# Performance work log

Hardware: AMD Instinct MI355X
Metric: run time of the kernel (lower is better)

## Reference

```python
import jax, jax.numpy as jnp
import numpy as np

T, B, N, DIN, H = 64, 32, 64, 128, 128  # seq_len, batch, num_nodes, input_dim, hid_dim
NUM_LAYERS = 2


def _make_cell_params(key, din):
    k1, k2, k3, k4 = jax.random.split(key, 4)
    s = 0.05
    Wg = jax.random.normal(k1, (2 * (din + H), 2 * H), jnp.float32) * s  # gates (r,u)
    bg = jnp.zeros((2 * H,), jnp.float32)
    Wc = jax.random.normal(k2, (2 * (din + H), H), jnp.float32) * s      # candidate
    bc = jnp.zeros((H,), jnp.float32)
    Wq = jax.random.normal(k3, (H, H), jnp.float32) * s                  # graph learner q
    Wk = jax.random.normal(k4, (H, H), jnp.float32) * s                  # graph learner k
    return Wg, bg, Wc, bc, Wq, Wk


def setup_inputs() -> dict:
    key = jax.random.key(0)
    k_in, k_sup, k_l0, k_l1 = jax.random.split(key, 4)
    inputs = jax.random.normal(k_in, (T, B, N, DIN), jnp.float32)
    initial_hidden_state = jnp.zeros((NUM_LAYERS, B, N * H), jnp.float32)
    supports = jax.nn.softmax(jax.random.normal(k_sup, (B, N, N), jnp.float32), axis=-1)
    Wg0, bg0, Wc0, bc0, Wq0, Wk0 = _make_cell_params(k_l0, DIN)
    Wg1, bg1, Wc1, bc1, Wq1, Wk1 = _make_cell_params(k_l1, H)
    return dict(inputs=inputs, initial_hidden_state=initial_hidden_state, supports=supports,
                Wg0=Wg0, bg0=bg0, Wc0=Wc0, bc0=bc0, Wq0=Wq0, Wk0=Wk0,
                Wg1=Wg1, bg1=bg1, Wc1=Wc1, bc1=bc1, Wq1=Wq1, Wk1=Wk1)


def _cell_step(params, supports, x, h):
    # x: (B, N, din), h: (B, N, H), supports: (B, N, N)
    Wg, bg, Wc, bc, Wq, Wk = params
    xh = jnp.concatenate([x, h], axis=-1)
    conv = jnp.einsum('bnm,bmd->bnd', supports, xh)                # graph conv
    gates = jax.nn.sigmoid(jnp.concatenate([xh, conv], -1) @ Wg + bg)
    r, u = jnp.split(gates, 2, axis=-1)
    xh_r = jnp.concatenate([x, r * h], axis=-1)
    conv_c = jnp.einsum('bnm,bmd->bnd', supports, xh_r)
    c = jnp.tanh(jnp.concatenate([xh_r, conv_c], -1) @ Wc + bc)
    h_new = u * h + (1.0 - u) * c
    # dynamic graph learner: new adjacency from the updated hidden state
    scores = jnp.einsum('bnd,bmd->bnm', h_new @ Wq, h_new @ Wk)
    new_supports = jax.nn.softmax(jax.nn.relu(scores), axis=-1)
    return h_new, new_supports


def _run_layer(params, x_seq, h0, supports, din):
    # x_seq: (T, B, N*din) -> hidden sequence (T, B, N, H)
    def step(carry, x_t):
        h, sup = carry
        h_new, sup_new = _cell_step(params, sup, x_t.reshape(B, N, din), h)
        return (h_new, sup_new), h_new
    (h_last, sup_last), hs = jax.lax.scan(step, (h0.reshape(B, N, H), supports), x_seq)
    return hs, h_last, sup_last


def reference(inputs, initial_hidden_state, supports,
              Wg0, bg0, Wc0, bc0, Wq0, Wk0,
              Wg1, bg1, Wc1, bc1, Wq1, Wk1):
    layer_params = [(Wg0, bg0, Wc0, bc0, Wq0, Wk0), (Wg1, bg1, Wc1, bc1, Wq1, Wk1)]
    dins = [DIN, H]
    cur = inputs.reshape(T, B, N * DIN)
    sup = supports
    out_hidden = []
    for i in range(NUM_LAYERS):
        hs, h_last, sup = _run_layer(layer_params[i], cur, initial_hidden_state[i], sup, dins[i])
        out_hidden.append(h_last.reshape(B, N * H))
        cur = hs.reshape(T, B, N * H)
    output_hidden = jnp.stack(out_hidden, axis=0)   # (num_layers, B, N*H)
    return output_hidden, cur                        # cur: (T, B, N*H)
```

## Files before the change

### kernel.cpp

```cpp
#include <hip/hip_runtime.h>

#define TT 64
#define BB 32
#define NN 64
#define HH 128
#define NH 8192

using short8 = __attribute__((ext_vector_type(8))) short;
using f32x16 = __attribute__((ext_vector_type(16))) float;

__device__ __forceinline__ unsigned short f2bf(float f) {
  unsigned int u = __float_as_uint(f);
  u = (u + 0x7FFFu + ((u >> 16) & 1u)) >> 16;
  return (unsigned short)u;
}
__device__ __forceinline__ float bf2f(unsigned short s) {
  return __uint_as_float(((unsigned int)s) << 16);
}
__device__ __forceinline__ float sigm(float x) { return 1.0f / (1.0f + __expf(-x)); }
__device__ __forceinline__ float tanh_fast(float x) { return 2.0f / (1.0f + __expf(-2.0f * x)) - 1.0f; }

__device__ __forceinline__ uint2 pack4(float a, float b, float c, float d) {
  uint2 r;
  r.x = (unsigned int)f2bf(a) | ((unsigned int)f2bf(b) << 16);
  r.y = (unsigned int)f2bf(c) | ((unsigned int)f2bf(d) << 16);
  return r;
}
__device__ __forceinline__ short8 ldsfrag(const unsigned short* p) {
  union { uint2 u2[2]; short8 s; } f;
  f.u2[0] = *(const uint2*)p;
  f.u2[1] = *(const uint2*)(p + 4);
  return f.s;
}
__device__ __forceinline__ short8 ldgfrag(const unsigned short* p) {
  union { uint4 u4; short8 s; } f;
  f.u4 = *(const uint4*)p;
  return f.s;
}

__global__ void sglc_pack(const float* __restrict__ Wg0, const float* __restrict__ Wc0,
                          const float* __restrict__ Wq0, const float* __restrict__ Wk0,
                          const float* __restrict__ Wg1, const float* __restrict__ Wc1,
                          const float* __restrict__ Wq1, const float* __restrict__ Wk1,
                          unsigned short* __restrict__ dst) {
  int idx = blockIdx.x * 256 + threadIdx.x;
  if (idx >= 458752) return;
  int layer = idx / 229376;
  int lo = idx - layer * 229376;
  const float* src; int nkc, ncshift, off;
  if (lo < 131072)      { src = layer ? Wg1 : Wg0; nkc = 32; ncshift = 8; off = 0; }
  else if (lo < 196608) { src = layer ? Wc1 : Wc0; nkc = 32; ncshift = 7; off = 131072; }
  else if (lo < 212992) { src = layer ? Wq1 : Wq0; nkc = 8;  ncshift = 7; off = 196608; }
  else                  { src = layer ? Wk1 : Wk0; nkc = 8;  ncshift = 7; off = 212992; }
  int l2 = lo - off;
  int k = l2 >> ncshift;
  int c = l2 & ((1 << ncshift) - 1);
  int c32 = c >> 5, n32 = c & 31;
  int kc = k >> 4, kl = k & 15;
  int half = kl >> 3, j = kl & 7;
  int lane = half * 32 + n32;
  int dstoff = layer * 229376 + off + (((c32 * nkc + kc) << 9) + lane * 8 + j);
  dst[dstoff] = f2bf(src[(size_t)k * (1 << ncshift) + c]);
}

#define SX_O   0
#define SH_O   8448
#define SRH_O  16896
#define SQ_O   25344
#define SK_O   33792
#define SSUP_O 42240
#define SPT_O  46592
#define LDS_USHORTS 64000

extern "C" __global__ void __launch_bounds__(1024, 4)
sglc_main(const float* __restrict__ Xin, const float* __restrict__ H0,
          const float* __restrict__ Sup0,
          const float* __restrict__ bg0, const float* __restrict__ bc0,
          const float* __restrict__ bg1, const float* __restrict__ bc1,
          const unsigned short* __restrict__ Wp, float* __restrict__ Out) {
  extern __shared__ unsigned short sm[];
  unsigned short* sX   = sm + SX_O;
  unsigned short* sHb  = sm + SH_O;
  unsigned short* sRH  = sm + SRH_O;
  unsigned short* sQ   = sm + SQ_O;
  unsigned short* sK   = sm + SK_O;
  unsigned short* sSup = sm + SSUP_O;
  unsigned short* sPT  = sm + SPT_O;
  float* sS = (float*)(sm + SPT_O);

  const int b = blockIdx.x;
  const int tid = threadIdx.x;
  const int lane = tid & 63;
  const int w = tid >> 6;
  const int n32 = lane & 31;
  const int half = lane >> 5;
  const int kob = half * 8;

  float* OutH = Out;
  float* Cur  = Out + 2 * BB * NH;

  float h_reg[32];

  for (int layer = 0; layer < 2; ++layer) {
    const int Lw = layer * 229376;
    const float* bg = layer ? bg1 : bg0;
    const float* bc = layer ? bc1 : bc0;
    const float* xbase = layer ? Cur : Xin;
    const float* h0p = H0 + (size_t)(layer * BB + b) * NH;

    const float bgv = (w < 8) ? bg[(w & 7) * 32 + n32] : 0.0f;
    const float bcv = (w >= 4 && w < 8) ? bc[(w - 4) * 32 + n32] : 0.0f;

    {
      int r = tid >> 4, c0 = (tid & 15) * 8;
      const float* hp = h0p + r * 128 + c0;
      float4 v0 = *(const float4*)(hp);
      float4 v1 = *(const float4*)(hp + 4);
      *(uint2*)(sHb + r * 132 + c0)     = pack4(v0.x, v0.y, v0.z, v0.w);
      *(uint2*)(sHb + r * 132 + c0 + 4) = pack4(v1.x, v1.y, v1.z, v1.w);
      const float* xp = xbase + (size_t)(0 * BB + b) * NH + r * 128 + c0;
      float4 x0 = *(const float4*)(xp);
      float4 x1 = *(const float4*)(xp + 4);
      *(uint2*)(sX + r * 132 + c0)     = pack4(x0.x, x0.y, x0.z, x0.w);
      *(uint2*)(sX + r * 132 + c0 + 4) = pack4(x1.x, x1.y, x1.z, x1.w);
      if (layer == 0) {
        int rs = tid >> 4, cs = (tid & 15) * 4;
        float4 sv = *(const float4*)(Sup0 + (size_t)b * 4096 + rs * 64 + cs);
        *(uint2*)(sSup + rs * 68 + cs) = pack4(sv.x, sv.y, sv.z, sv.w);
      }
    }
    if (w >= 4 && w < 8) {
      const int col = (w - 4) * 32 + n32;
#pragma unroll
      for (int tt = 0; tt < 2; ++tt)
#pragma unroll
        for (int g = 0; g < 4; ++g)
#pragma unroll
          for (int i = 0; i < 4; ++i)
            h_reg[tt * 16 + 4 * g + i] = h0p[(tt * 32 + 8 * g + 4 * half + i) * 128 + col];
    }
    __syncthreads();

    for (int t = 0; t < TT; ++t) {
      union { float u[32]; short8 bq[8]; } su_;
      f32x16 acc0, acc1;
#pragma unroll
      for (int z = 0; z < 16; ++z) { acc0[z] = 0.0f; acc1[z] = 0.0f; }

      {
        const int c32g = w & 7;
        const unsigned short* wb = Wp + Lw + (((c32g * 32 + (w < 8 ? 0 : 16)) << 9) + lane * 8);
#pragma unroll
        for (int kc = 0; kc < 16; ++kc) {
          const unsigned short* asrc = (kc < 8) ? (sX + kc * 16 + kob) : (sHb + (kc - 8) * 16 + kob);
          short8 a0 = ldsfrag(asrc + n32 * 132);
          short8 a1 = ldsfrag(asrc + (32 + n32) * 132);
          short8 bf = ldgfrag(wb + (kc << 9));
          acc0 = __builtin_amdgcn_mfma_f32_32x32x16_bf16(a0, bf, acc0, 0, 0, 0);
          acc1 = __builtin_amdgcn_mfma_f32_32x32x16_bf16(a1, bf, acc1, 0, 0, 0);
        }
        if (w >= 8) {
          unsigned short* pb = sPT + (c32g * 32 + n32) * 68;
#pragma unroll
          for (int tt = 0; tt < 2; ++tt) {
            const f32x16& ac = tt ? acc1 : acc0;
#pragma unroll
            for (int g = 0; g < 4; ++g)
              *(uint2*)(pb + tt * 32 + 8 * g + 4 * half) =
                  pack4(ac[4 * g], ac[4 * g + 1], ac[4 * g + 2], ac[4 * g + 3]);
          }
        }
      }
      __syncthreads();

      if (w < 8) {
        const int c32g = w & 7;
#pragma unroll
        for (int kc2 = 0; kc2 < 4; ++kc2) {
          short8 a0 = ldsfrag(sSup + n32 * 68 + kc2 * 16 + kob);
          short8 a1 = ldsfrag(sSup + (32 + n32) * 68 + kc2 * 16 + kob);
          short8 bf = ldsfrag(sPT + (c32g * 32 + n32) * 68 + kc2 * 16 + kob);
          acc0 = __builtin_amdgcn_mfma_f32_32x32x16_bf16(a0, bf, acc0, 0, 0, 0);
          acc1 = __builtin_amdgcn_mfma_f32_32x32x16_bf16(a1, bf, acc1, 0, 0, 0);
        }
        const int col = (w & 7) * 32 + n32;
        if (w < 4) {
#pragma unroll
          for (int tt = 0; tt < 2; ++tt) {
            const f32x16& ac = tt ? acc1 : acc0;
#pragma unroll
            for (int g = 0; g < 4; ++g)
#pragma unroll
              for (int i = 0; i < 4; ++i) {
                int row = tt * 32 + 8 * g + 4 * half + i;
                float rv = sigm(ac[4 * g + i] + bgv);
                float hv = bf2f(sHb[row * 132 + col]);
                sRH[row * 132 + col] = f2bf(rv * hv);
              }
          }
        } else {
#pragma unroll
          for (int tt = 0; tt < 2; ++tt) {
            const f32x16& ac = tt ? acc1 : acc0;
#pragma unroll
            for (int g = 0; g < 4; ++g)
#pragma unroll
              for (int i = 0; i < 4; ++i)
                su_.u[tt * 16 + 4 * g + i] = sigm(ac[4 * g + i] + bgv);
          }
        }
      } else {
        const unsigned short* qb =
            Wp + Lw + ((w < 12) ? 196608 : 212992) + ((((w - 8) & 3) * 8) << 9) + lane * 8;
#pragma unroll
        for (int kc = 0; kc < 8; ++kc) su_.bq[kc] = ldgfrag(qb + (kc << 9));
      }
      __syncthreads();

      f32x16 ca0, ca1;
#pragma unroll
      for (int z = 0; z < 16; ++z) { ca0[z] = 0.0f; ca1[z] = 0.0f; }
      if (w >= 4 && w < 12) {
        const int c32c = (w < 8) ? (w - 4) : (w - 8);
        const unsigned short* wb = Wp + Lw + 131072 + (((c32c * 32 + (w < 8 ? 0 : 16)) << 9) + lane * 8);
#pragma unroll
        for (int kc = 0; kc < 16; ++kc) {
          const unsigned short* asrc = (kc < 8) ? (sX + kc * 16 + kob) : (sRH + (kc - 8) * 16 + kob);
          short8 a0 = ldsfrag(asrc + n32 * 132);
          short8 a1 = ldsfrag(asrc + (32 + n32) * 132);
          short8 bf = ldgfrag(wb + (kc << 9));
          ca0 = __builtin_amdgcn_mfma_f32_32x32x16_bf16(a0, bf, ca0, 0, 0, 0);
          ca1 = __builtin_amdgcn_mfma_f32_32x32x16_bf16(a1, bf, ca1, 0, 0, 0);
        }
        if (w >= 8) {
          unsigned short* pb = sPT + (c32c * 32 + n32) * 68;
#pragma unroll
          for (int tt = 0; tt < 2; ++tt) {
            const f32x16& ac = tt ? ca1 : ca0;
#pragma unroll
            for (int g = 0; g < 4; ++g)
              *(uint2*)(pb + tt * 32 + 8 * g + 4 * half) =
                  pack4(ac[4 * g], ac[4 * g + 1], ac[4 * g + 2], ac[4 * g + 3]);
          }
        }
      }
      __syncthreads();

      if (w >= 4 && w < 8) {
        const int c32c = w - 4;
        const int col = c32c * 32 + n32;
#pragma unroll
        for (int kc2 = 0; kc2 < 4; ++kc2) {
          short8 a0 = ldsfrag(sSup + n32 * 68 + kc2 * 16 + kob);
          short8 a1 = ldsfrag(sSup + (32 + n32) * 68 + kc2 * 16 + kob);
          short8 bf = ldsfrag(sPT + col * 68 + kc2 * 16 + kob);
          ca0 = __builtin_amdgcn_mfma_f32_32x32x16_bf16(a0, bf, ca0, 0, 0, 0);
          ca1 = __builtin_amdgcn_mfma_f32_32x32x16_bf16(a1, bf, ca1, 0, 0, 0);
        }
        float* curp = Cur + (size_t)(t * BB + b) * NH;
        float* outp = OutH + (size_t)(layer * BB + b) * NH;
#pragma unroll
        for (int tt = 0; tt < 2; ++tt) {
          const f32x16& ac = tt ? ca1 : ca0;
#pragma unroll
          for (int g = 0; g < 4; ++g)
#pragma unroll
            for (int i = 0; i < 4; ++i) {
              int r16 = tt * 16 + 4 * g + i;
              float cv = tanh_fast(ac[4 * g + i] + bcv);
              float uv = su_.u[r16];
              float hn = uv * h_reg[r16] + (1.0f - uv) * cv;
              h_reg[r16] = hn;
              int row = tt * 32 + 8 * g + 4 * half + i;
              sHb[row * 132 + col] = f2bf(hn);
              curp[row * 128 + col] = hn;
              if (t == TT - 1) outp[row * 128 + col] = hn;
            }
        }
      } else if (w < 4 || w >= 12) {
        if (t < TT - 1) {
          const float* xn = xbase + (size_t)((t + 1) * BB + b) * NH;
          int sidx = (w < 4 ? w : w - 8) * 64 + lane;
          int r = sidx >> 3, c0 = (sidx & 7) * 16;
          const float* sp = xn + r * 128 + c0;
          unsigned short* dp = sX + r * 132 + c0;
#pragma unroll
          for (int q4 = 0; q4 < 4; ++q4) {
            float4 v = *(const float4*)(sp + q4 * 4);
            *(uint2*)(dp + q4 * 4) = pack4(v.x, v.y, v.z, v.w);
          }
        }
      }
      __syncthreads();

      if (w >= 8) {
        const int col = ((w - 8) & 3) * 32 + n32;
        f32x16 qa0, qa1;
#pragma unroll
        for (int z = 0; z < 16; ++z) { qa0[z] = 0.0f; qa1[z] = 0.0f; }
#pragma unroll
        for (int kc = 0; kc < 8; ++kc) {
          short8 a0 = ldsfrag(sHb + n32 * 132 + kc * 16 + kob);
          short8 a1 = ldsfrag(sHb + (32 + n32) * 132 + kc * 16 + kob);
          qa0 = __builtin_amdgcn_mfma_f32_32x32x16_bf16(a0, su_.bq[kc], qa0, 0, 0, 0);
          qa1 = __builtin_amdgcn_mfma_f32_32x32x16_bf16(a1, su_.bq[kc], qa1, 0, 0, 0);
        }
        unsigned short* dstm = (w < 12) ? sQ : sK;
#pragma unroll
        for (int tt = 0; tt < 2; ++tt) {
          const f32x16& ac = tt ? qa1 : qa0;
#pragma unroll
          for (int g = 0; g < 4; ++g)
#pragma unroll
            for (int i = 0; i < 4; ++i)
              dstm[(tt * 32 + 8 * g + 4 * half + i) * 132 + col] = f2bf(ac[4 * g + i]);
        }
      }
      __syncthreads();

      if (w < 4) {
        const int rt = w & 1, ct = w >> 1;
        f32x16 sa;
#pragma unroll
        for (int z = 0; z < 16; ++z) sa[z] = 0.0f;
#pragma unroll
        for (int kc = 0; kc < 8; ++kc) {
          short8 a0 = ldsfrag(sQ + (rt * 32 + n32) * 132 + kc * 16 + kob);
          short8 bf = ldsfrag(sK + (ct * 32 + n32) * 132 + kc * 16 + kob);
          sa = __builtin_amdgcn_mfma_f32_32x32x16_bf16(a0, bf, sa, 0, 0, 0);
        }
#pragma unroll
        for (int g = 0; g < 4; ++g)
#pragma unroll
          for (int i = 0; i < 4; ++i)
            sS[(rt * 32 + 8 * g + 4 * half + i) * 66 + ct * 32 + n32] = fmaxf(sa[4 * g + i], 0.0f);
      }
      __syncthreads();

      {
        int row = tid >> 4, ci = (tid & 15) * 4;
        float2 v01 = *(const float2*)(sS + row * 66 + ci);
        float2 v23 = *(const float2*)(sS + row * 66 + ci + 2);
        float s0 = v01.x, s1 = v01.y, s2 = v23.x, s3 = v23.y;
        float mx = fmaxf(fmaxf(s0, s1), fmaxf(s2, s3));
#pragma unroll
        for (int off = 1; off < 16; off <<= 1) mx = fmaxf(mx, __shfl_xor(mx, off, 16));
        float e0 = __expf(s0 - mx), e1 = __expf(s1 - mx);
        float e2 = __expf(s2 - mx), e3 = __expf(s3 - mx);
        float sum = e0 + e1 + e2 + e3;
#pragma unroll
        for (int off = 1; off < 16; off <<= 1) sum += __shfl_xor(sum, off, 16);
        float inv = 1.0f / sum;
        *(uint2*)(sSup + row * 68 + ci) = pack4(e0 * inv, e1 * inv, e2 * inv, e3 * inv);
      }
      __syncthreads();
    }
    __syncthreads();
  }
}

extern "C" void kernel_launch(void* const* d_in, const int* in_sizes, int n_in,
                              void* d_out, int out_size, void* d_ws, size_t ws_size,
                              hipStream_t stream) {
  const float* Xin  = (const float*)d_in[0];
  const float* H0   = (const float*)d_in[1];
  const float* Sup0 = (const float*)d_in[2];
  const float* Wg0  = (const float*)d_in[3];
  const float* bg0  = (const float*)d_in[4];
  const float* Wc0  = (const float*)d_in[5];
  const float* bc0  = (const float*)d_in[6];
  const float* Wq0  = (const float*)d_in[7];
  const float* Wk0  = (const float*)d_in[8];
  const float* Wg1  = (const float*)d_in[9];
  const float* bg1  = (const float*)d_in[10];
  const float* Wc1  = (const float*)d_in[11];
  const float* bc1  = (const float*)d_in[12];
  const float* Wq1  = (const float*)d_in[13];
  const float* Wk1  = (const float*)d_in[14];
  unsigned short* Wp = (unsigned short*)d_ws;

  hipFuncSetAttribute(reinterpret_cast<const void*>(sglc_main),
                      hipFuncAttributeMaxDynamicSharedMemorySize, LDS_USHORTS * 2);

  hipLaunchKernelGGL(sglc_pack, dim3(1792), dim3(256), 0, stream,
                     Wg0, Wc0, Wq0, Wk0, Wg1, Wc1, Wq1, Wk1, Wp);
  hipLaunchKernelGGL(sglc_main, dim3(BB), dim3(1024), LDS_USHORTS * 2, stream,
                     Xin, H0, Sup0, bg0, bc0, bg1, bc1, Wp, (float*)d_out);
}
```

Measured before the change: 3.456 ms.

## Precompute input projections in parallel kernel and keep recurrent weights in registers

Result: slower. 3.725 ms (+7.8%).

```diff
diff --git a/kernel.cpp b/kernel.cpp
--- a/kernel.cpp
+++ b/kernel.cpp
@@ -3,7 +3,6 @@
 #define TT 64
 #define BB 32
 #define NN 64
-#define HH 128
 #define NH 8192
 
 using short8 = __attribute__((ext_vector_type(8))) short;
@@ -14,18 +13,18 @@
   u = (u + 0x7FFFu + ((u >> 16) & 1u)) >> 16;
   return (unsigned short)u;
 }
+__device__ __forceinline__ unsigned int pack2(float a, float b) {
+  return (unsigned int)f2bf(a) | ((unsigned int)f2bf(b) << 16);
+}
+__device__ __forceinline__ uint2 pack4(float a, float b, float c, float d) {
+  uint2 r; r.x = pack2(a, b); r.y = pack2(c, d); return r;
+}
 __device__ __forceinline__ float bf2f(unsigned short s) {
   return __uint_as_float(((unsigned int)s) << 16);
 }
 __device__ __forceinline__ float sigm(float x) { return 1.0f / (1.0f + __expf(-x)); }
 __device__ __forceinline__ float tanh_fast(float x) { return 2.0f / (1.0f + __expf(-2.0f * x)) - 1.0f; }
 
-__device__ __forceinline__ uint2 pack4(float a, float b, float c, float d) {
-  uint2 r;
-  r.x = (unsigned int)f2bf(a) | ((unsigned int)f2bf(b) << 16);
-  r.y = (unsigned int)f2bf(c) | ((unsigned int)f2bf(d) << 16);
-  return r;
-}
 __device__ __forceinline__ short8 ldsfrag(const unsigned short* p) {
   union { uint2 u2[2]; short8 s; } f;
   f.u2[0] = *(const uint2*)p;
@@ -36,6 +35,22 @@
   union { uint4 u4; short8 s; } f;
   f.u4 = *(const uint4*)p;
   return f.s;
+}
+__device__ __forceinline__ void store16(unsigned short* p, const f32x16& v) {
+  uint4 q0, q1;
+  q0.x = pack2(v[0], v[1]);   q0.y = pack2(v[2], v[3]);
+  q0.z = pack2(v[4], v[5]);   q0.w = pack2(v[6], v[7]);
+  q1.x = pack2(v[8], v[9]);   q1.y = pack2(v[10], v[11]);
+  q1.z = pack2(v[12], v[13]); q1.w = pack2(v[14], v[15]);
+  *(uint4*)p = q0; *(uint4*)(p + 8) = q1;
+}
+__device__ __forceinline__ void addinit(f32x16& a, uint4 c0, uint4 c1) {
+  unsigned int u[8] = {c0.x, c0.y, c0.z, c0.w, c1.x, c1.y, c1.z, c1.w};
+#pragma unroll
+  for (int i = 0; i < 8; ++i) {
+    a[2 * i]     += __uint_as_float(u[i] << 16);
+    a[2 * i + 1] += __uint_as_float(u[i] & 0xffff0000u);
+  }
 }
 
 __global__ void sglc_pack(const float* __restrict__ Wg0, const float* __restrict__ Wc0,
@@ -46,316 +61,356 @@
   int idx = blockIdx.x * 256 + threadIdx.x;
   if (idx >= 458752) return;
   int layer = idx / 229376;
-  int lo = idx - layer * 229376;
-  const float* src; int nkc, ncshift, off;
-  if (lo < 131072)      { src = layer ? Wg1 : Wg0; nkc = 32; ncshift = 8; off = 0; }
-  else if (lo < 196608) { src = layer ? Wc1 : Wc0; nkc = 32; ncshift = 7; off = 131072; }
-  else if (lo < 212992) { src = layer ? Wq1 : Wq0; nkc = 8;  ncshift = 7; off = 196608; }
-  else                  { src = layer ? Wk1 : Wk0; nkc = 8;  ncshift = 7; off = 212992; }
-  int l2 = lo - off;
-  int k = l2 >> ncshift;
-  int c = l2 & ((1 << ncshift) - 1);
-  int c32 = c >> 5, n32 = c & 31;
-  int kc = k >> 4, kl = k & 15;
-  int half = kl >> 3, j = kl & 7;
-  int lane = half * 32 + n32;
-  int dstoff = layer * 229376 + off + (((c32 * nkc + kc) << 9) + lane * 8 + j);
-  dst[dstoff] = f2bf(src[(size_t)k * (1 << ncshift) + c]);
-}
-
-#define SX_O   0
-#define SH_O   8448
-#define SRH_O  16896
-#define SQ_O   25344
-#define SK_O   33792
-#define SSUP_O 42240
-#define SPT_O  46592
-#define LDS_USHORTS 64000
-
-extern "C" __global__ void __launch_bounds__(1024, 4)
-sglc_main(const float* __restrict__ Xin, const float* __restrict__ H0,
-          const float* __restrict__ Sup0,
-          const float* __restrict__ bg0, const float* __restrict__ bc0,
-          const float* __restrict__ bg1, const float* __restrict__ bc1,
-          const unsigned short* __restrict__ Wp, float* __restrict__ Out) {
+  int l = idx - layer * 229376;
+  const float* Wg = layer ? Wg1 : Wg0;
+  const float* Wc = layer ? Wc1 : Wc0;
+  const float* Wq = layer ? Wq1 : Wq0;
+  const float* Wk = layer ? Wk1 : Wk0;
+  int region = (l < 98304) ? 0 : 1;
+  int l2 = region ? (l - 98304) : l;
+  int tile = l2 >> 12;
+  int rem = l2 & 4095;
+  int kc = rem >> 9, li = rem & 511;
+  int lane = li >> 3, jj = li & 7;
+  int krow = kc * 16 + (lane >> 5) * 8 + jj;
+  int col32 = lane & 31;
+  const float* src; int ld, row0, colbase;
+  if (region == 0) {
+    if (tile < 8)       { src = Wg; ld = 256; row0 = 0;   colbase = tile * 32; }
+    else if (tile < 16) { src = Wg; ld = 256; row0 = 256; colbase = (tile - 8) * 32; }
+    else if (tile < 20) { src = Wc; ld = 128; row0 = 0;   colbase = (tile - 16) * 32; }
+    else                { src = Wc; ld = 128; row0 = 256; colbase = (tile - 20) * 32; }
+  } else {
+    if (tile < 8)       { src = Wg; ld = 256; row0 = 128; colbase = tile * 32; }
+    else if (tile < 16) { src = Wg; ld = 256; row0 = 384; colbase = (tile - 8) * 32; }
+    else if (tile < 20) { src = Wc; ld = 128; row0 = 128; colbase = (tile - 16) * 32; }
+    else if (tile < 24) { src = Wc; ld = 128; row0 = 384; colbase = (tile - 20) * 32; }
+    else if (tile < 28) { src = Wq; ld = 128; row0 = 0;   colbase = (tile - 24) * 32; }
+    else                { src = Wk; ld = 128; row0 = 0;   colbase = (tile - 28) * 32; }
+  }
+  dst[idx] = f2bf(src[(size_t)(row0 + krow) * ld + colbase + col32]);
+}
+
+__global__ void __launch_bounds__(256)
+sglc_pre(const float* __restrict__ xbase, const unsigned short* __restrict__ Wpre,
+         unsigned short* __restrict__ Pinit) {
+  const int gw = blockIdx.x * 4 + (threadIdx.x >> 6);
+  const int lane = threadIdx.x & 63;
+  const int n32 = lane & 31, half = lane >> 5;
+  const int t = gw >> 5, b = gw & 31;
+  const float* xp = xbase + (size_t)(t * BB + b) * NH;
+  short8 afr[2][8];
+#pragma unroll
+  for (int rt = 0; rt < 2; ++rt)
+#pragma unroll
+    for (int kc = 0; kc < 8; ++kc) {
+      const float* s = xp + (size_t)(rt * 32 + n32) * 128 + kc * 16 + half * 8;
+      float4 v0 = *(const float4*)s;
+      float4 v1 = *(const float4*)(s + 4);
+      union { uint2 u[2]; short8 ss; } tmp;
+      tmp.u[0] = pack4(v0.x, v0.y, v0.z, v0.w);
+      tmp.u[1] = pack4(v1.x, v1.y, v1.z, v1.w);
+      afr[rt][kc] = tmp.ss;
+    }
+  unsigned short* ob = Pinit + ((size_t)(t * BB + b) * 24) * 2048;
+  for (int j = 0; j < 24; ++j) {
+    f32x16 a0, a1;
+#pragma unroll
+    for (int z = 0; z < 16; ++z) { a0[z] = 0.0f; a1[z] = 0.0f; }
+#pragma unroll
+    for (int kc = 0; kc < 8; ++kc) {
+      short8 bf = ldgfrag(Wpre + ((j * 8 + kc) << 9) + lane * 8);
+      a0 = __builtin_amdgcn_mfma_f32_32x32x16_bf16(afr[0][kc], bf, a0, 0, 0, 0);
+      a1 = __builtin_amdgcn_mfma_f32_32x32x16_bf16(afr[1][kc], bf, a1, 0, 0, 0);
+    }
+    store16(ob + (j * 2 + 0) * 1024 + lane * 16, a0);
+    store16(ob + (j * 2 + 1) * 1024 + lane * 16, a1);
+  }
+}
+
+#define SHB_O  0
+#define SRH_O  8448
+#define SSUP_O 16896
+#define SPT_O  21248
+#define SQ_O   21248
+#define SK_O   29696
+#define SS_O   38656
+#define SHF_O  47104
+#define SU_O   63744
+#define LDS_BYTES 160768
+
+__global__ void __launch_bounds__(1024, 4)
+sglc_rec(const float* __restrict__ H0l, const float* __restrict__ Sup0,
+         const unsigned short* __restrict__ SupX,
+         const float* __restrict__ bg, const float* __restrict__ bc,
+         const unsigned short* __restrict__ Wrec, const unsigned short* __restrict__ Pinit,
+         unsigned short* __restrict__ SupXout,
+         float* __restrict__ OutHl, float* __restrict__ Cur, int layer) {
   extern __shared__ unsigned short sm[];
-  unsigned short* sX   = sm + SX_O;
-  unsigned short* sHb  = sm + SH_O;
+  unsigned short* sHb  = sm + SHB_O;
   unsigned short* sRH  = sm + SRH_O;
+  unsigned short* sSup = sm + SSUP_O;
+  unsigned short* sPT  = sm + SPT_O;
   unsigned short* sQ   = sm + SQ_O;
   unsigned short* sK   = sm + SK_O;
-  unsigned short* sSup = sm + SSUP_O;
-  unsigned short* sPT  = sm + SPT_O;
-  float* sS = (float*)(sm + SPT_O);
-
-  const int b = blockIdx.x;
-  const int tid = threadIdx.x;
-  const int lane = tid & 63;
-  const int w = tid >> 6;
-  const int n32 = lane & 31;
-  const int half = lane >> 5;
-  const int kob = half * 8;
-
-  float* OutH = Out;
-  float* Cur  = Out + 2 * BB * NH;
-
-  float h_reg[32];
-
-  for (int layer = 0; layer < 2; ++layer) {
-    const int Lw = layer * 229376;
-    const float* bg = layer ? bg1 : bg0;
-    const float* bc = layer ? bc1 : bc0;
-    const float* xbase = layer ? Cur : Xin;
-    const float* h0p = H0 + (size_t)(layer * BB + b) * NH;
-
-    const float bgv = (w < 8) ? bg[(w & 7) * 32 + n32] : 0.0f;
-    const float bcv = (w >= 4 && w < 8) ? bc[(w - 4) * 32 + n32] : 0.0f;
-
+  float* sS  = (float*)(sm + SS_O);
+  float* sHf = (float*)(sm + SHF_O);
+  float* sU  = (float*)(sm + SU_O);
+
+  const int b = blockIdx.x, tid = threadIdx.x;
+  const int lane = tid & 63, w = tid >> 6;
+  const int n32 = lane & 31, half = lane >> 5, kob = half * 8;
+
+  short8 wg[8];
+#pragma unroll
+  for (int kc = 0; kc < 8; ++kc)
+    wg[kc] = ldgfrag(Wrec + ((w * 8 + kc) << 9) + lane * 8);
+
+  const float bgv = (w < 8) ? bg[w * 32 + n32] : 0.0f;
+  const float bcv = (w >= 4 && w < 8) ? bc[(w - 4) * 32 + n32] : 0.0f;
+
+  {
+    int r = tid >> 4, c0 = (tid & 15) * 8;
+    const float* hp = H0l + (size_t)b * NH + r * 128 + c0;
+    float4 v0 = *(const float4*)(hp);
+    float4 v1 = *(const float4*)(hp + 4);
+    sHf[r * 130 + c0 + 0] = v0.x; sHf[r * 130 + c0 + 1] = v0.y;
+    sHf[r * 130 + c0 + 2] = v0.z; sHf[r * 130 + c0 + 3] = v0.w;
+    sHf[r * 130 + c0 + 4] = v1.x; sHf[r * 130 + c0 + 5] = v1.y;
+    sHf[r * 130 + c0 + 6] = v1.z; sHf[r * 130 + c0 + 7] = v1.w;
+    *(uint2*)(sHb + r * 132 + c0)     = pack4(v0.x, v0.y, v0.z, v0.w);
+    *(uint2*)(sHb + r * 132 + c0 + 4) = pack4(v1.x, v1.y, v1.z, v1.w);
+    if (layer == 0) {
+      int cs = (tid & 15) * 4;
+      float4 sv = *(const float4*)(Sup0 + (size_t)b * 4096 + r * 64 + cs);
+      *(uint2*)(sSup + r * 68 + cs) = pack4(sv.x, sv.y, sv.z, sv.w);
+    } else {
+      for (int i = tid; i < 4352; i += 1024) sSup[i] = SupX[(size_t)b * 4352 + i];
+    }
+  }
+  __syncthreads();
+
+  for (int t = 0; t < TT; ++t) {
+    const size_t pbase = ((size_t)(t * BB + b) * 24) * 2048;
+
+    f32x16 acc0, acc1;
     {
-      int r = tid >> 4, c0 = (tid & 15) * 8;
-      const float* hp = h0p + r * 128 + c0;
-      float4 v0 = *(const float4*)(hp);
-      float4 v1 = *(const float4*)(hp + 4);
-      *(uint2*)(sHb + r * 132 + c0)     = pack4(v0.x, v0.y, v0.z, v0.w);
-      *(uint2*)(sHb + r * 132 + c0 + 4) = pack4(v1.x, v1.y, v1.z, v1.w);
-      const float* xp = xbase + (size_t)(0 * BB + b) * NH + r * 128 + c0;
-      float4 x0 = *(const float4*)(xp);
-      float4 x1 = *(const float4*)(xp + 4);
-      *(uint2*)(sX + r * 132 + c0)     = pack4(x0.x, x0.y, x0.z, x0.w);
-      *(uint2*)(sX + r * 132 + c0 + 4) = pack4(x1.x, x1.y, x1.z, x1.w);
-      if (layer == 0) {
-        int rs = tid >> 4, cs = (tid & 15) * 4;
-        float4 sv = *(const float4*)(Sup0 + (size_t)b * 4096 + rs * 64 + cs);
-        *(uint2*)(sSup + rs * 68 + cs) = pack4(sv.x, sv.y, sv.z, sv.w);
-      }
+      const unsigned short* pb = Pinit + pbase + (size_t)w * 2048 + lane * 16;
+      uint4 c00 = *(const uint4*)(pb);
+      uint4 c01 = *(const uint4*)(pb + 8);
+      uint4 c10 = *(const uint4*)(pb + 1024);
+      uint4 c11 = *(const uint4*)(pb + 1024 + 8);
+#pragma unroll
+      for (int z = 0; z < 16; ++z) { acc0[z] = 0.0f; acc1[z] = 0.0f; }
+#pragma unroll
+      for (int kc = 0; kc < 8; ++kc) {
+        short8 a0 = ldsfrag(sHb + n32 * 132 + kc * 16 + kob);
+        short8 a1 = ldsfrag(sHb + (32 + n32) * 132 + kc * 16 + kob);
+        acc0 = __builtin_amdgcn_mfma_f32_32x32x16_bf16(a0, wg[kc], acc0, 0, 0, 0);
+        acc1 = __builtin_amdgcn_mfma_f32_32x32x16_bf16(a1, wg[kc], acc1, 0, 0, 0);
+      }
+      addinit(acc0, c00, c01);
+      addinit(acc1, c10, c11);
+      if (w >= 8) {
+        unsigned short* pt = sPT + ((w - 8) * 32 + n32) * 68;
+#pragma unroll
+        for (int tt = 0; tt < 2; ++tt) {
+          const f32x16& ac = tt ? acc1 : acc0;
+#pragma unroll
+          for (int g = 0; g < 4; ++g)
+            *(uint2*)(pt + tt * 32 + 8 * g + 4 * half) =
+                pack4(ac[4 * g], ac[4 * g + 1], ac[4 * g + 2], ac[4 * g + 3]);
+        }
+      }
+    }
+    __syncthreads();
+
+    short8 st[8];
+    if (w >= 4 && w < 12) {
+      const int tile = w + 12;
+#pragma unroll
+      for (int kc = 0; kc < 8; ++kc)
+        st[kc] = ldgfrag(Wrec + ((tile * 8 + kc) << 9) + lane * 8);
+    }
+    if (w < 8) {
+#pragma unroll
+      for (int kc2 = 0; kc2 < 4; ++kc2) {
+        short8 a0 = ldsfrag(sSup + n32 * 68 + kc2 * 16 + kob);
+        short8 a1 = ldsfrag(sSup + (32 + n32) * 68 + kc2 * 16 + kob);
+        short8 bf = ldsfrag(sPT + (w * 32 + n32) * 68 + kc2 * 16 + kob);
+        acc0 = __builtin_amdgcn_mfma_f32_32x32x16_bf16(a0, bf, acc0, 0, 0, 0);
+        acc1 = __builtin_amdgcn_mfma_f32_32x32x16_bf16(a1, bf, acc1, 0, 0, 0);
+      }
+      const int col = w * 32 + n32;
+      if (w < 4) {
+#pragma unroll
+        for (int tt = 0; tt < 2; ++tt) {
+          const f32x16& ac = tt ? acc1 : acc0;
+#pragma unroll
+          for (int g = 0; g < 4; ++g)
+#pragma unroll
+            for (int i = 0; i < 4; ++i) {
+              int row = tt * 32 + 8 * g + 4 * half + i;
+              float rv = sigm(ac[4 * g + i] + bgv);
+              sRH[row * 132 + col] = f2bf(rv * sHf[row * 130 + col]);
+            }
+        }
+      } else {
+        const int ucol = col - 128;
+#pragma unroll
+        for (int tt = 0; tt < 2; ++tt) {
+          const f32x16& ac = tt ? acc1 : acc0;
+#pragma unroll
+          for (int g = 0; g < 4; ++g)
+#pragma unroll
+            for (int i = 0; i < 4; ++i) {
+              int row = tt * 32 + 8 * g + 4 * half + i;
+              sU[row * 130 + ucol] = sigm(ac[4 * g + i] + bgv);
+            }
+        }
+      }
+    }
+    __syncthreads();
+
+    f32x16 ca0, ca1;
+    if (w >= 4 && w < 12) {
+      const unsigned short* pb = Pinit + pbase + (size_t)(w + 12) * 2048 + lane * 16;
+      uint4 c00 = *(const uint4*)(pb);
+      uint4 c01 = *(const uint4*)(pb + 8);
+      uint4 c10 = *(const uint4*)(pb + 1024);
+      uint4 c11 = *(const uint4*)(pb + 1024 + 8);
+#pragma unroll
+      for (int z = 0; z < 16; ++z) { ca0[z] = 0.0f; ca1[z] = 0.0f; }
+#pragma unroll
+      for (int kc = 0; kc < 8; ++kc) {
+        short8 a0 = ldsfrag(sRH + n32 * 132 + kc * 16 + kob);
+        short8 a1 = ldsfrag(sRH + (32 + n32) * 132 + kc * 16 + kob);
+        ca0 = __builtin_amdgcn_mfma_f32_32x32x16_bf16(a0, st[kc], ca0, 0, 0, 0);
+        ca1 = __builtin_amdgcn_mfma_f32_32x32x16_bf16(a1, st[kc], ca1, 0, 0, 0);
+      }
+      addinit(ca0, c00, c01);
+      addinit(ca1, c10, c11);
+      if (w >= 8) {
+        unsigned short* pt = sPT + ((w - 8) * 32 + n32) * 68;
+#pragma unroll
+        for (int tt = 0; tt < 2; ++tt) {
+          const f32x16& ac = tt ? ca1 : ca0;
+#pragma unroll
+          for (int g = 0; g < 4; ++g)
+            *(uint2*)(pt + tt * 32 + 8 * g + 4 * half) =
+                pack4(ac[4 * g], ac[4 * g + 1], ac[4 * g + 2], ac[4 * g + 3]);
+        }
+      }
+    }
+    __syncthreads();
+
+    if (w < 4) {
+#pragma unroll
+      for (int kc = 0; kc < 8; ++kc)
+        st[kc] = ldgfrag(Wrec + (((24 + w) * 8 + kc) << 9) + lane * 8);
+    } else if (w >= 12) {
+#pragma unroll
+      for (int kc = 0; kc < 8; ++kc)
+        st[kc] = ldgfrag(Wrec + (((16 + w) * 8 + kc) << 9) + lane * 8);
     }
     if (w >= 4 && w < 8) {
       const int col = (w - 4) * 32 + n32;
 #pragma unroll
-      for (int tt = 0; tt < 2; ++tt)
+      for (int kc2 = 0; kc2 < 4; ++kc2) {
+        short8 a0 = ldsfrag(sSup + n32 * 68 + kc2 * 16 + kob);
+        short8 a1 = ldsfrag(sSup + (32 + n32) * 68 + kc2 * 16 + kob);
+        short8 bf = ldsfrag(sPT + ((w - 4) * 32 + n32) * 68 + kc2 * 16 + kob);
+        ca0 = __builtin_amdgcn_mfma_f32_32x32x16_bf16(a0, bf, ca0, 0, 0, 0);
+        ca1 = __builtin_amdgcn_mfma_f32_32x32x16_bf16(a1, bf, ca1, 0, 0, 0);
+      }
+      float* curp = Cur + (size_t)(t * BB + b) * NH;
+      float* outp = OutHl + (size_t)b * NH;
+#pragma unroll
+      for (int tt = 0; tt < 2; ++tt) {
+        const f32x16& ac = tt ? ca1 : ca0;
 #pragma unroll
         for (int g = 0; g < 4; ++g)
 #pragma unroll
+          for (int i = 0; i < 4; ++i) {
+            int row = tt * 32 + 8 * g + 4 * half + i;
+            float cv = tanh_fast(ac[4 * g + i] + bcv);
+            float uv = sU[row * 130 + col];
+            float hn = uv * sHf[row * 130 + col] + (1.0f - uv) * cv;
+            sHf[row * 130 + col] = hn;
+            sHb[row * 132 + col] = f2bf(hn);
+            curp[row * 128 + col] = hn;
+            if (t == TT - 1) outp[row * 128 + col] = hn;
+          }
+      }
+    }
+    __syncthreads();
+
+    if (w < 4 || w >= 12) {
+      f32x16 qa0, qa1;
+#pragma unroll
+      for (int z = 0; z < 16; ++z) { qa0[z] = 0.0f; qa1[z] = 0.0f; }
+#pragma unroll
+      for (int kc = 0; kc < 8; ++kc) {
+        short8 a0 = ldsfrag(sHb + n32 * 132 + kc * 16 + kob);
+        short8 a1 = ldsfrag(sHb + (32 + n32) * 132 + kc * 16 + kob);
+        qa0 = __builtin_amdgcn_mfma_f32_32x32x16_bf16(a0, st[kc], qa0, 0, 0, 0);
+        qa1 = __builtin_amdgcn_mfma_f32_32x32x16_bf16(a1, st[kc], qa1, 0, 0, 0);
+      }
+      unsigned short* dq = (w < 4) ? sQ : sK;
+      const int col = (w < 4 ? w : w - 12) * 32 + n32;
+#pragma unroll
+      for (int tt = 0; tt < 2; ++tt) {
+        const f32x16& ac = tt ? qa1 : qa0;
+#pragma unroll
+        for (int g = 0; g < 4; ++g)
+#pragma unroll
           for (int i = 0; i < 4; ++i)
-            h_reg[tt * 16 + 4 * g + i] = h0p[(tt * 32 + 8 * g + 4 * half + i) * 128 + col];
-    }
-    __syncthreads();
-
-    for (int t = 0; t < TT; ++t) {
-      union { float u[32]; short8 bq[8]; } su_;
-      f32x16 acc0, acc1;
-#pragma unroll
-      for (int z = 0; z < 16; ++z) { acc0[z] = 0.0f; acc1[z] = 0.0f; }
-
-      {
-        const int c32g = w & 7;
-        const unsigned short* wb = Wp + Lw + (((c32g * 32 + (w < 8 ? 0 : 16)) << 9) + lane * 8);
-#pragma unroll
-        for (int kc = 0; kc < 16; ++kc) {
-          const unsigned short* asrc = (kc < 8) ? (sX + kc * 16 + kob) : (sHb + (kc - 8) * 16 + kob);
-          short8 a0 = ldsfrag(asrc + n32 * 132);
-          short8 a1 = ldsfrag(asrc + (32 + n32) * 132);
-          short8 bf = ldgfrag(wb + (kc << 9));
-          acc0 = __builtin_amdgcn_mfma_f32_32x32x16_bf16(a0, bf, acc0, 0, 0, 0);
-          acc1 = __builtin_amdgcn_mfma_f32_32x32x16_bf16(a1, bf, acc1, 0, 0, 0);
-        }
-        if (w >= 8) {
-          unsigned short* pb = sPT + (c32g * 32 + n32) * 68;
-#pragma unroll
-          for (int tt = 0; tt < 2; ++tt) {
-            const f32x16& ac = tt ? acc1 : acc0;
-#pragma unroll
-            for (int g = 0; g < 4; ++g)
-              *(uint2*)(pb + tt * 32 + 8 * g + 4 * half) =
-                  pack4(ac[4 * g], ac[4 * g + 1], ac[4 * g + 2], ac[4 * g + 3]);
-          }
-        }
-      }
-      __syncthreads();
-
-      if (w < 8) {
-        const int c32g = w & 7;
-#pragma unroll
-        for (int kc2 = 0; kc2 < 4; ++kc2) {
-          short8 a0 = ldsfrag(sSup + n32 * 68 + kc2 * 16 + kob);
-          short8 a1 = ldsfrag(sSup + (32 + n32) * 68 + kc2 * 16 + kob);
-          short8 bf = ldsfrag(sPT + (c32g * 32 + n32) * 68 + kc2 * 16 + kob);
-          acc0 = __builtin_amdgcn_mfma_f32_32x32x16_bf16(a0, bf, acc0, 0, 0, 0);
-          acc1 = __builtin_amdgcn_mfma_f32_32x32x16_bf16(a1, bf, acc1, 0, 0, 0);
-        }
-        const int col = (w & 7) * 32 + n32;
-        if (w < 4) {
-#pragma unroll
-          for (int tt = 0; tt < 2; ++tt) {
-            const f32x16& ac = tt ? acc1 : acc0;
-#pragma unroll
-            for (int g = 0; g < 4; ++g)
-#pragma unroll
-              for (int i = 0; i < 4; ++i) {
-                int row = tt * 32 + 8 * g + 4 * half + i;
-                float rv = sigm(ac[4 * g + i] + bgv);
-                float hv = bf2f(sHb[row * 132 + col]);
-                sRH[row * 132 + col] = f2bf(rv * hv);
-              }
-          }
-        } else {
-#pragma unroll
-          for (int tt = 0; tt < 2; ++tt) {
-            const f32x16& ac = tt ? acc1 : acc0;
-#pragma unroll
-            for (int g = 0; g < 4; ++g)
-#pragma unroll
-              for (int i = 0; i < 4; ++i)
-                su_.u[tt * 16 + 4 * g + i] = sigm(ac[4 * g + i] + bgv);
-          }
-        }
-      } else {
-        const unsigned short* qb =
-            Wp + Lw + ((w < 12) ? 196608 : 212992) + ((((w - 8) & 3) * 8) << 9) + lane * 8;
-#pragma unroll
-        for (int kc = 0; kc < 8; ++kc) su_.bq[kc] = ldgfrag(qb + (kc << 9));
-      }
-      __syncthreads();
-
-      f32x16 ca0, ca1;
-#pragma unroll
-      for (int z = 0; z < 16; ++z) { ca0[z] = 0.0f; ca1[z] = 0.0f; }
-      if (w >= 4 && w < 12) {
-        const int c32c = (w < 8) ? (w - 4) : (w - 8);
-        const unsigned short* wb = Wp + Lw + 131072 + (((c32c * 32 + (w < 8 ? 0 : 16)) << 9) + lane * 8);
-#pragma unroll
-        for (int kc = 0; kc < 16; ++kc) {
-          const unsigned short* asrc = (kc < 8) ? (sX + kc * 16 + kob) : (sRH + (kc - 8) * 16 + kob);
-          short8 a0 = ldsfrag(asrc + n32 * 132);
-          short8 a1 = ldsfrag(asrc + (32 + n32) * 132);
-          short8 bf = ldgfrag(wb + (kc << 9));
-          ca0 = __builtin_amdgcn_mfma_f32_32x32x16_bf16(a0, bf, ca0, 0, 0, 0);
-          ca1 = __builtin_amdgcn_mfma_f32_32x32x16_bf16(a1, bf, ca1, 0, 0, 0);
-        }
-        if (w >= 8) {
-          unsigned short* pb = sPT + (c32c * 32 + n32) * 68;
-#pragma unroll
-          for (int tt = 0; tt < 2; ++tt) {
-            const f32x16& ac = tt ? ca1 : ca0;
-#pragma unroll
-            for (int g = 0; g < 4; ++g)
-              *(uint2*)(pb + tt * 32 + 8 * g + 4 * half) =
-                  pack4(ac[4 * g], ac[4 * g + 1], ac[4 * g + 2], ac[4 * g + 3]);
-          }
-        }
-      }
-      __syncthreads();
-
-      if (w >= 4 && w < 8) {
-        const int c32c = w - 4;
-        const int col = c32c * 32 + n32;
-#pragma unroll
-        for (int kc2 = 0; kc2 < 4; ++kc2) {
-          short8 a0 = ldsfrag(sSup + n32 * 68 + kc2 * 16 + kob);
-          short8 a1 = ldsfrag(sSup + (32 + n32) * 68 + kc2 * 16 + kob);
-          short8 bf = ldsfrag(sPT + col * 68 + kc2 * 16 + kob);
-          ca0 = __builtin_amdgcn_mfma_f32_32x32x16_bf16(a0, bf, ca0, 0, 0, 0);
-          ca1 = __builtin_amdgcn_mfma_f32_32x32x16_bf16(a1, bf, ca1, 0, 0, 0);
-        }
-        float* curp = Cur + (size_t)(t * BB + b) * NH;
-        float* outp = OutH + (size_t)(layer * BB + b) * NH;
-#pragma unroll
-        for (int tt = 0; tt < 2; ++tt) {
-          const f32x16& ac = tt ? ca1 : ca0;
-#pragma unroll
-          for (int g = 0; g < 4; ++g)
-#pragma unroll
-            for (int i = 0; i < 4; ++i) {
-              int r16 = tt * 16 + 4 * g + i;
-              float cv = tanh_fast(ac[4 * g + i] + bcv);
-              float uv = su_.u[r16];
-              float hn = uv * h_reg[r16] + (1.0f - uv) * cv;
-              h_reg[r16] = hn;
-              int row = tt * 32 + 8 * g + 4 * half + i;
-              sHb[row * 132 + col] = f2bf(hn);
-              curp[row * 128 + col] = hn;
-              if (t == TT - 1) outp[row * 128 + col] = hn;
-            }
-        }
-      } else if (w < 4 || w >= 12) {
-        if (t < TT - 1) {
-          const float* xn = xbase + (size_t)((t + 1) * BB + b) * NH;
-          int sidx = (w < 4 ? w : w - 8) * 64 + lane;
-          int r = sidx >> 3, c0 = (sidx & 7) * 16;
-          const float* sp = xn + r * 128 + c0;
-          unsigned short* dp = sX + r * 132 + c0;
-#pragma unroll
-          for (int q4 = 0; q4 < 4; ++q4) {
-            float4 v = *(const float4*)(sp + q4 * 4);
-            *(uint2*)(dp + q4 * 4) = pack4(v.x, v.y, v.z, v.w);
-          }
-        }
-      }
-      __syncthreads();
-
-      if (w >= 8) {
-        const int col = ((w - 8) & 3) * 32 + n32;
-        f32x16 qa0, qa1;
-#pragma unroll
-        for (int z = 0; z < 16; ++z) { qa0[z] = 0.0f; qa1[z] = 0.0f; }
-#pragma unroll
-        for (int kc = 0; kc < 8; ++kc) {
-          short8 a0 = ldsfrag(sHb + n32 * 132 + kc * 16 + kob);
-          short8 a1 = ldsfrag(sHb + (32 + n32) * 132 + kc * 16 + kob);
-          qa0 = __builtin_amdgcn_mfma_f32_32x32x16_bf16(a0, su_.bq[kc], qa0, 0, 0, 0);
-          qa1 = __builtin_amdgcn_mfma_f32_32x32x16_bf16(a1, su_.bq[kc], qa1, 0, 0, 0);
-        }
-        unsigned short* dstm = (w < 12) ? sQ : sK;
-#pragma unroll
-        for (int tt = 0; tt < 2; ++tt) {
-          const f32x16& ac = tt ? qa1 : qa0;
-#pragma unroll
-          for (int g = 0; g < 4; ++g)
-#pragma unroll
-            for (int i = 0; i < 4; ++i)
-              dstm[(tt * 32 + 8 * g + 4 * half + i) * 132 + col] = f2bf(ac[4 * g + i]);
-        }
-      }
-      __syncthreads();
-
-      if (w < 4) {
-        const int rt = w & 1, ct = w >> 1;
-        f32x16 sa;
-#pragma unroll
-        for (int z = 0; z < 16; ++z) sa[z] = 0.0f;
-#pragma unroll
-        for (int kc = 0; kc < 8; ++kc) {
-          short8 a0 = ldsfrag(sQ + (rt * 32 + n32) * 132 + kc * 16 + kob);
-          short8 bf = ldsfrag(sK + (ct * 32 + n32) * 132 + kc * 16 + kob);
-          sa = __builtin_amdgcn_mfma_f32_32x32x16_bf16(a0, bf, sa, 0, 0, 0);
-        }
-#pragma unroll
-        for (int g = 0; g < 4; ++g)
-#pragma unroll
-          for (int i = 0; i < 4; ++i)
-            sS[(rt * 32 + 8 * g + 4 * half + i) * 66 + ct * 32 + n32] = fmaxf(sa[4 * g + i], 0.0f);
-      }
-      __syncthreads();
-
-      {
-        int row = tid >> 4, ci = (tid & 15) * 4;
-        float2 v01 = *(const float2*)(sS + row * 66 + ci);
-        float2 v23 = *(const float2*)(sS + row * 66 + ci + 2);
-        float s0 = v01.x, s1 = v01.y, s2 = v23.x, s3 = v23.y;
-        float mx = fmaxf(fmaxf(s0, s1), fmaxf(s2, s3));
-#pragma unroll
-        for (int off = 1; off < 16; off <<= 1) mx = fmaxf(mx, __shfl_xor(mx, off, 16));
-        float e0 = __expf(s0 - mx), e1 = __expf(s1 - mx);
-        float e2 = __expf(s2 - mx), e3 = __expf(s3 - mx);
-        float sum = e0 + e1 + e2 + e3;
-#pragma unroll
-        for (int off = 1; off < 16; off <<= 1) sum += __shfl_xor(sum, off, 16);
-        float inv = 1.0f / sum;
-        *(uint2*)(sSup + row * 68 + ci) = pack4(e0 * inv, e1 * inv, e2 * inv, e3 * inv);
-      }
-      __syncthreads();
-    }
-    __syncthreads();
+            dq[(tt * 32 + 8 * g + 4 * half + i) * 132 + col] = f2bf(ac[4 * g + i]);
+      }
+    }
+    __syncthreads();
+
+    if (w < 4) {
+      const int rt = w & 1, ct = w >> 1;
+      f32x16 sa;
+#pragma unroll
+      for (int z = 0; z < 16; ++z) sa[z] = 0.0f;
+#pragma unroll
+      for (int kc = 0; kc < 8; ++kc) {
+        short8 a0 = ldsfrag(sQ + (rt * 32 + n32) * 132 + kc * 16 + kob);
+        short8 bf = ldsfrag(sK + (ct * 32 + n32) * 132 + kc * 16 + kob);
+        sa = __builtin_amdgcn_mfma_f32_32x32x16_bf16(a0, bf, sa, 0, 0, 0);
+      }
+#pragma unroll
+      for (int g = 0; g < 4; ++g)
+#pragma unroll
+        for (int i = 0; i < 4; ++i)
+          sS[(rt * 32 + 8 * g + 4 * half + i) * 66 + ct * 32 + n32] =
+              fmaxf(sa[4 * g + i], 0.0f);
+    }
+    __syncthreads();
+
+    {
+      int row = tid >> 4, ci = (tid & 15) * 4;
+      float2 v01 = *(const float2*)(sS + row * 66 + ci);
+      float2 v23 = *(const float2*)(sS + row * 66 + ci + 2);
+      float s0 = v01.x, s1 = v01.y, s2 = v23.x, s3 = v23.y;
+      float mx = fmaxf(fmaxf(s0, s1), fmaxf(s2, s3));
+#pragma unroll
+      for (int off = 1; off < 16; off <<= 1) mx = fmaxf(mx, __shfl_xor(mx, off, 16));
+      float e0 = __expf(s0 - mx), e1 = __expf(s1 - mx);
+      float e2 = __expf(s2 - mx), e3 = __expf(s3 - mx);
+      float sum = e0 + e1 + e2 + e3;
+#pragma unroll
+      for (int off = 1; off < 16; off <<= 1) sum += __shfl_xor(sum, off, 16);
+      float inv = 1.0f / sum;
+      *(uint2*)(sSup + row * 68 + ci) = pack4(e0 * inv, e1 * inv, e2 * inv, e3 * inv);
+    }
+    __syncthreads();
+  }
+
+  if (layer == 0) {
+    for (int i = tid; i < 4352; i += 1024) SupXout[(size_t)b * 4352 + i] = sSup[i];
   }
 }
 
@@ -377,13 +432,26 @@
   const float* bc1  = (const float*)d_in[12];
   const float* Wq1  = (const float*)d_in[13];
   const float* Wk1  = (const float*)d_in[14];
-  unsigned short* Wp = (unsigned short*)d_ws;
-
-  hipFuncSetAttribute(reinterpret_cast<const void*>(sglc_main),
-                      hipFuncAttributeMaxDynamicSharedMemorySize, LDS_USHORTS * 2);
+
+  if (ws_size < 202522624ull) return;
+  unsigned short* Wp    = (unsigned short*)d_ws;
+  unsigned short* Pinit = Wp + 458752;
+  unsigned short* SupX  = Pinit + 100663296;
+
+  float* Out = (float*)d_out;
+  float* Cur = Out + 2 * BB * NH;
+
+  hipFuncSetAttribute(reinterpret_cast<const void*>(sglc_rec),
+                      hipFuncAttributeMaxDynamicSharedMemorySize, LDS_BYTES);
 
   hipLaunchKernelGGL(sglc_pack, dim3(1792), dim3(256), 0, stream,
                      Wg0, Wc0, Wq0, Wk0, Wg1, Wc1, Wq1, Wk1, Wp);
-  hipLaunchKernelGGL(sglc_main, dim3(BB), dim3(1024), LDS_USHORTS * 2, stream,
-                     Xin, H0, Sup0, bg0, bc0, bg1, bc1, Wp, (float*)d_out);
-}
+  hipLaunchKernelGGL(sglc_pre, dim3(512), dim3(256), 0, stream, Xin, Wp, Pinit);
+  hipLaunchKernelGGL(sglc_rec, dim3(BB), dim3(1024), LDS_BYTES, stream,
+                     H0, Sup0, SupX, bg0, bc0, Wp + 98304, Pinit, SupX,
+                     Out, Cur, 0);
+  hipLaunchKernelGGL(sglc_pre, dim3(512), dim3(256), 0, stream, Cur, Wp + 229376, Pinit);
+  hipLaunchKernelGGL(sglc_rec, dim3(BB), dim3(1024), LDS_BYTES, stream,
+                     H0 + BB * NH, Sup0, SupX, bg1, bc1, Wp + 229376 + 98304, Pinit, SupX,
+                     Out + BB * NH, Cur, 1);
+}
```
